# Optimization experiments

Measured on AMD Instinct MI355X. Metric: run time of the kernel, lower is better.

The kernel has to match this reference:

```python
import jax, jax.numpy as jnp
import numpy as np
from jax import lax

EPS_ACT = 1e-5
EPS_RMS = 1e-6


def _ste(x, q):
    # straight-through estimator: forward = q, backward = identity
    return x + lax.stop_gradient(q - x)


def _act_quant8(x):
    # per-last-dim symmetric 8-bit activation quantization (BitNet style)
    scale = 127.0 / jnp.clip(jnp.max(jnp.abs(x), axis=-1, keepdims=True), EPS_ACT)
    return jnp.clip(jnp.round(x * scale), -128.0, 127.0) / scale


def _w_quant_8bit(w):
    # per-tensor symmetric 8-bit weight quantization
    scale = 127.0 / jnp.clip(jnp.max(jnp.abs(w)), EPS_ACT)
    return jnp.clip(jnp.round(w * scale), -128.0, 127.0) / scale


def _w_quant_binary(w):
    # per-tensor binary: sign(w) * mean(|w|)
    return jnp.sign(w) * jnp.mean(jnp.abs(w))


def _rmsnorm(x):
    return x * lax.rsqrt(jnp.mean(x * x, axis=-1, keepdims=True) + EPS_RMS)


def _bit_conv(x, w, quant_type, groups):
    xq = _ste(x, _act_quant8(x))
    wq = _ste(w, _w_quant_binary(w) if quant_type == 'Binary' else _w_quant_8bit(w))
    return lax.conv_general_dilated(
        xq, wq, window_strides=(1, 1), padding='VALID',
        feature_group_count=groups,
        dimension_numbers=('NCHW', 'OIHW', 'NCHW'))


def _bit_linear(x, w):
    x = _rmsnorm(x)                       # NormType='RMS' (no learned scale)
    xq = _ste(x, _act_quant8(x))
    wq = _ste(w, _w_quant_binary(w))      # QuantType='Binary', per-tensor
    return xq @ wq.T


def setup_inputs() -> dict:
    key = jax.random.key(0)
    ks = jax.random.split(key, 8)
    B = 8192
    return {
        'x':        jax.random.normal(ks[0], (B, 1, 16, 16), jnp.float32),
        'w_conv1':  jax.random.normal(ks[1], (16, 1, 3, 3),  jnp.float32) * 0.1,
        'w_conv1b': jax.random.normal(ks[2], (16, 16, 3, 3), jnp.float32) * 0.1,
        'w_conv2':  jax.random.normal(ks[3], (96, 1, 12, 12), jnp.float32) * 0.1,
        'w_fc1':    jax.random.normal(ks[4], (64, 96), jnp.float32) * 0.1,
        'w_fc2':    jax.random.normal(ks[5], (64, 64), jnp.float32) * 0.1,
        'w_fc3':    jax.random.normal(ks[6], (64, 64), jnp.float32) * 0.1,
        'w_fcl':    jax.random.normal(ks[7], (10, 64), jnp.float32) * 0.1,
    }


def reference(x, w_conv1, w_conv1b, w_conv2, w_fc1, w_fc2, w_fc3, w_fcl):
    h = jax.nn.relu(_bit_conv(x, w_conv1, '8bit', 1))        # [B,16,14,14]
    h = jax.nn.relu(_bit_conv(h, w_conv1b, '8bit', 1))       # [B,16,12,12]
    h = jax.nn.relu(_bit_conv(h, w_conv2, 'Binary', 16))     # [B,96,1,1]
    h = h.reshape(h.shape[0], -1)                            # [B,96]
    h = jax.nn.relu(_bit_linear(h, w_fc1))                   # [B,64]
    h = jax.nn.relu(_bit_linear(h, w_fc2))                   # [B,64]
    h = jax.nn.relu(_bit_linear(h, w_fc3))                   # [B,64]
    return _bit_linear(h, w_fcl)                             # [B,10]
```

## Files before the change

kernel.cpp:

```cpp
#include <hip/hip_runtime.h>
#include <math.h>


#define OFF_W1   0
#define OFF_W1B  192
#define OFF_W2   3264
#define OFF_F1   17088
#define OFF_F2   23232
#define OFF_F3   27328
#define OFF_FL   31424

#define EPS_TIE  3e-5f

__device__ __forceinline__ float quantq(float v, float s) {
    const float u  = __fmul_rn(v, s);
    const float fl = floorf(u);
    const float fr = __fsub_rn(u, fl);
    float q;
    if (fabsf(__fsub_rn(fr, 0.5f)) < EPS_TIE) q = __fadd_rn(fl, 0.5f);
    else                                      q = rintf(u);
    q = fminf(q, 127.f);
    return __fdiv_rn(q, s);
}

__device__ __forceinline__ float leaf_abs_sum(const float* __restrict__ p, int n) {
    float r[8];
    #pragma unroll
    for (int j = 0; j < 8; ++j) r[j] = fabsf(p[j]);
    const int nb = n & ~7;
    for (int i = 8; i < nb; i += 8) {
        #pragma unroll
        for (int j = 0; j < 8; ++j) r[j] = __fadd_rn(r[j], fabsf(p[i + j]));
    }
    float c = __fadd_rn(__fadd_rn(__fadd_rn(r[0], r[1]), __fadd_rn(r[2], r[3])),
                        __fadd_rn(__fadd_rn(r[4], r[5]), __fadd_rn(r[6], r[7])));
    for (int i = nb; i < n; ++i) c = __fadd_rn(c, fabsf(p[i]));
    return c;
}

__global__ __launch_bounds__(256) void wq_kernel(
    const float* __restrict__ w1, const float* __restrict__ w1b,
    const float* __restrict__ w2, const float* __restrict__ f1,
    const float* __restrict__ f2, const float* __restrict__ f3,
    const float* __restrict__ fl, float* __restrict__ ws)
{
    __shared__ float red[256];
    __shared__ float ls[128];
    const int blk = blockIdx.x, t = threadIdx.x;

    const float* src; int n; int mode; int off; int K; int W;
    switch (blk) {
        case 0:  src = w1;  n = 144;   mode = 0; off = OFF_W1;  K = 0;   W = 0;  break;
        case 1:  src = w1b; n = 2304;  mode = 0; off = OFF_W1B; K = 0;   W = 0;  break;
        case 2:  src = w2;  n = 13824; mode = 1; off = OFF_W2;  K = 144; W = 96; break;
        case 3:  src = f1;  n = 6144;  mode = 1; off = OFF_F1;  K = 96;  W = 64; break;
        case 4:  src = f2;  n = 4096;  mode = 1; off = OFF_F2;  K = 64;  W = 64; break;
        case 5:  src = f3;  n = 4096;  mode = 1; off = OFF_F3;  K = 64;  W = 64; break;
        default: src = fl;  n = 640;   mode = 1; off = OFF_FL;  K = 64;  W = 10; break;
    }

    if (mode == 0) {
        float p = 0.f;
        for (int i = t; i < n; i += 256) p = fmaxf(p, fabsf(src[i]));
        red[t] = p;
        __syncthreads();
        for (int s = 128; s > 0; s >>= 1) {
            if (t < s) red[t] = fmaxf(red[t], red[t + s]);
            __syncthreads();
        }
        const float s = __fdiv_rn(127.0f, fmaxf(red[0], 1e-5f));
        for (int i = t; i < n; i += 256) {
            float q = rintf(__fmul_rn(src[i], s));
            q = fminf(fmaxf(q, -128.f), 127.f);
            int d;
            if (blk == 0) d = (i / 9) * 12 + (i % 9);
            else          { const int oc = i / 144, k = i % 144;
                            d = oc * 192 + (k / 9) * 12 + (k % 9); }
            ws[off + d] = __fdiv_rn(q, s);
        }
    } else {
        int nleaf, loff, lsz;
        switch (n) {
            case 13824: nleaf = 128; loff = (t >> 1) * 216 + (t & 1) * 104;
                        lsz = (t & 1) ? 112 : 104; break;
            case 6144:  nleaf = 64;  loff = t * 96;  lsz = 96;  break;
            case 4096:  nleaf = 32;  loff = t * 128; lsz = 128; break;
            default:    nleaf = 8;   loff = t * 80;  lsz = 80;  break;
        }
        if (t < nleaf) ls[t] = leaf_abs_sum(src + loff, lsz);
        __syncthreads();
        for (int m = nleaf >> 1; m >= 1; m >>= 1) {
            float v = 0.f;
            if (t < m) v = __fadd_rn(ls[2 * t], ls[2 * t + 1]);
            __syncthreads();
            if (t < m) ls[t] = v;
            __syncthreads();
        }
        const float alpha = __fdiv_rn(ls[0], (float)n);
        for (int i = t; i < n; i += 256) {
            const float w = src[i];
            const float sg = (w > 0.f) ? 1.f : ((w < 0.f) ? -1.f : 0.f);
            const int d = (i % K) * W + (i / K);
            ws[off + d] = __fmul_rn(sg, alpha);
        }
    }
}

__global__ __launch_bounds__(256, 8) void fused_kernel(
    const float* __restrict__ x, const float* __restrict__ ws,
    float* __restrict__ out)
{
    __shared__ __align__(16) float s_x[16][20];
    __shared__ __align__(16) float s_h1[16][14][20];
    __shared__ float s_h2[16 * 156];
    __shared__ float s_v96[96];
    __shared__ float s_t96[96];
    __shared__ float s_q[96];
    __shared__ float s_r8[8];

    const int b = blockIdx.x;
    const int t = threadIdx.x;

    {
        const float v = x[b * 256 + t];
        float m = fabsf(v);
        #pragma unroll
        for (int msk = 8; msk >= 1; msk >>= 1) m = fmaxf(m, __shfl_xor(m, msk, 16));
        const float s = __fdiv_rn(127.0f, fmaxf(m, 1e-5f));
        float q = rintf(__fmul_rn(v, s));
        q = fminf(fmaxf(q, -128.f), 127.f);
        s_x[t >> 4][t & 15] = __fdiv_rn(q, s);
    }
    __syncthreads();

    if (t < 224) {
        const int oc = t / 14, oh = t % 14;
        const float* __restrict__ wg = ws + OFF_W1 + oc * 12;
        const float4 wv0 = *(const float4*)&wg[0];
        const float4 wv1 = *(const float4*)&wg[4];
        const float  w8  = wg[8];
        const float wr[9] = {wv0.x, wv0.y, wv0.z, wv0.w,
                             wv1.x, wv1.y, wv1.z, wv1.w, w8};
        float acc[14];
        #pragma unroll
        for (int ow = 0; ow < 14; ++ow) acc[ow] = 0.f;
        #pragma unroll
        for (int kh = 0; kh < 3; ++kh) {
            float A[16];
            *(float4*)&A[0]  = *(const float4*)&s_x[oh + kh][0];
            *(float4*)&A[4]  = *(const float4*)&s_x[oh + kh][4];
            *(float4*)&A[8]  = *(const float4*)&s_x[oh + kh][8];
            *(float4*)&A[12] = *(const float4*)&s_x[oh + kh][12];
            #pragma unroll
            for (int kw = 0; kw < 3; ++kw) {
                const float wk = wr[kh * 3 + kw];
                #pragma unroll
                for (int ow = 0; ow < 14; ++ow)
                    acc[ow] = __fmaf_rn(A[ow + kw], wk, acc[ow]);
            }
        }
        float mx = 0.f;
        #pragma unroll
        for (int ow = 0; ow < 14; ++ow) { acc[ow] = fmaxf(acc[ow], 0.f); mx = fmaxf(mx, acc[ow]); }
        const float s = __fdiv_rn(127.0f, fmaxf(mx, 1e-5f));
        float q[14];
        #pragma unroll
        for (int ow = 0; ow < 14; ++ow) q[ow] = quantq(acc[ow], s);
        *(float4*)&s_h1[oc][oh][0]  = *(const float4*)&q[0];
        *(float4*)&s_h1[oc][oh][4]  = *(const float4*)&q[4];
        *(float4*)&s_h1[oc][oh][8]  = *(const float4*)&q[8];
        *(float2*)&s_h1[oc][oh][12] = *(const float2*)&q[12];
    }
    __syncthreads();

    if (t < 192) {
        const int oc = t / 12, oh = t % 12;
        const float* __restrict__ wg = ws + OFF_W1B + oc * 192;
        float acc[12];
        #pragma unroll
        for (int i = 0; i < 12; ++i) acc[i] = 0.f;
        for (int ic = 0; ic < 16; ++ic) {
            const float4 wv0 = *(const float4*)&wg[ic * 12];
            const float4 wv1 = *(const float4*)&wg[ic * 12 + 4];
            const float  w8  = wg[ic * 12 + 8];
            const float wr[9] = {wv0.x, wv0.y, wv0.z, wv0.w,
                                 wv1.x, wv1.y, wv1.z, wv1.w, w8};
            #pragma unroll
            for (int kh = 0; kh < 3; ++kh) {
                float A[14];
                *(float4*)&A[0]  = *(const float4*)&s_h1[ic][oh + kh][0];
                *(float4*)&A[4]  = *(const float4*)&s_h1[ic][oh + kh][4];
                *(float4*)&A[8]  = *(const float4*)&s_h1[ic][oh + kh][8];
                *(float2*)&A[12] = *(const float2*)&s_h1[ic][oh + kh][12];
                #pragma unroll
                for (int kw = 0; kw < 3; ++kw) {
                    const float w = wr[kh * 3 + kw];
                    #pragma unroll
                    for (int ow = 0; ow < 12; ++ow)
                        acc[ow] = __fmaf_rn(A[ow + kw], w, acc[ow]);
                }
            }
        }
        float mx = 0.f;
        #pragma unroll
        for (int ow = 0; ow < 12; ++ow) { acc[ow] = fmaxf(acc[ow], 0.f); mx = fmaxf(mx, acc[ow]); }
        const float s = __fdiv_rn(127.0f, fmaxf(mx, 1e-5f));
        const int hb = oc * 156 + oh * 13;
        #pragma unroll
        for (int ow = 0; ow < 12; ++ow)
            s_h2[hb + ow] = quantq(acc[ow], s);
    }
    __syncthreads();

    if (t < 96) {
        const int g = t / 6;
        const float* __restrict__ wp = ws + OFF_W2;
        float acc = 0.f;
        #pragma unroll
        for (int r = 0; r < 12; ++r) {
            const int hb = g * 156 + r * 13;
            #pragma unroll
            for (int c = 0; c < 12; ++c)
                acc = __fmaf_rn(s_h2[hb + c], wp[(r * 12 + c) * 96 + t], acc);
        }
        s_v96[t] = fmaxf(acc, 0.f);
    }
    __syncthreads();

    if (t >= 64) return;

    float u;
    {
        const float va = s_v96[t];
        const float vb = (t < 32) ? s_v96[64 + t] : 0.f;
        s_t96[t] = __fmul_rn(va, va);
        if (t < 32) s_t96[64 + t] = __fmul_rn(vb, vb);
        if (t < 8) {
            float r = s_t96[t];
            for (int i = 8; i < 96; i += 8) r = __fadd_rn(r, s_t96[i + t]);
            s_r8[t] = r;
        }
        const float c = __fadd_rn(
            __fadd_rn(__fadd_rn(s_r8[0], s_r8[1]), __fadd_rn(s_r8[2], s_r8[3])),
            __fadd_rn(__fadd_rn(s_r8[4], s_r8[5]), __fadd_rn(s_r8[6], s_r8[7])));
        const float mean = __fdiv_rn(c, 96.0f);
        const float bc1 = __fdiv_rn(1.0f, __fsqrt_rn(__fadd_rn(mean, 1e-6f)));
        const float n0 = __fmul_rn(va, bc1);
        const float n1 = __fmul_rn(vb, bc1);
        float m = n0;
        if (t < 32) m = fmaxf(m, n1);
        #pragma unroll
        for (int msk = 32; msk >= 1; msk >>= 1) m = fmaxf(m, __shfl_xor(m, msk, 64));
        const float s2 = __fdiv_rn(127.0f, fmaxf(m, 1e-5f));
        s_q[t] = quantq(n0, s2);
        if (t < 32) s_q[64 + t] = quantq(n1, s2);
        const float* __restrict__ wp = ws + OFF_F1;
        float acc = 0.f;
        for (int k = 0; k < 96; ++k) acc = __fmaf_rn(s_q[k], wp[k * 64 + t], acc);
        u = fmaxf(acc, 0.f);
    }

    #pragma unroll 1
    for (int stage = 0; stage < 2; ++stage) {
        const int woff = stage == 0 ? OFF_F2 : OFF_F3;
        s_t96[t] = __fmul_rn(u, u);
        if (t < 8) {
            float r = s_t96[t];
            for (int i = 8; i < 64; i += 8) r = __fadd_rn(r, s_t96[i + t]);
            s_r8[t] = r;
        }
        const float c = __fadd_rn(
            __fadd_rn(__fadd_rn(s_r8[0], s_r8[1]), __fadd_rn(s_r8[2], s_r8[3])),
            __fadd_rn(__fadd_rn(s_r8[4], s_r8[5]), __fadd_rn(s_r8[6], s_r8[7])));
        const float mean = __fdiv_rn(c, 64.0f);
        const float bc1 = __fdiv_rn(1.0f, __fsqrt_rn(__fadd_rn(mean, 1e-6f)));
        const float n0 = __fmul_rn(u, bc1);
        float m = n0;
        #pragma unroll
        for (int msk = 32; msk >= 1; msk >>= 1) m = fmaxf(m, __shfl_xor(m, msk, 64));
        const float s2 = __fdiv_rn(127.0f, fmaxf(m, 1e-5f));
        s_q[t] = quantq(n0, s2);
        const float* __restrict__ wp = ws + woff;
        float acc = 0.f;
        for (int k = 0; k < 64; ++k) acc = __fmaf_rn(s_q[k], wp[k * 64 + t], acc);
        u = fmaxf(acc, 0.f);
    }

    {
        s_t96[t] = __fmul_rn(u, u);
        if (t < 8) {
            float r = s_t96[t];
            for (int i = 8; i < 64; i += 8) r = __fadd_rn(r, s_t96[i + t]);
            s_r8[t] = r;
        }
        const float c = __fadd_rn(
            __fadd_rn(__fadd_rn(s_r8[0], s_r8[1]), __fadd_rn(s_r8[2], s_r8[3])),
            __fadd_rn(__fadd_rn(s_r8[4], s_r8[5]), __fadd_rn(s_r8[6], s_r8[7])));
        const float mean = __fdiv_rn(c, 64.0f);
        const float bc1 = __fdiv_rn(1.0f, __fsqrt_rn(__fadd_rn(mean, 1e-6f)));
        const float n0 = __fmul_rn(u, bc1);
        float m = n0;
        #pragma unroll
        for (int msk = 32; msk >= 1; msk >>= 1) m = fmaxf(m, __shfl_xor(m, msk, 64));
        const float s2 = __fdiv_rn(127.0f, fmaxf(m, 1e-5f));
        s_q[t] = quantq(n0, s2);
        const int to = (t < 10) ? t : 9;
        const float* __restrict__ wp = ws + OFF_FL;
        float acc = 0.f;
        for (int k = 0; k < 64; ++k) acc = __fmaf_rn(s_q[k], wp[k * 10 + to], acc);
        if (t < 10) out[b * 10 + t] = acc;
    }
}

extern "C" void kernel_launch(void* const* d_in, const int* in_sizes, int n_in,
                              void* d_out, int out_size, void* d_ws, size_t ws_size,
                              hipStream_t stream) {
    const float* x   = (const float*)d_in[0];
    const float* w1  = (const float*)d_in[1];
    const float* w1b = (const float*)d_in[2];
    const float* w2  = (const float*)d_in[3];
    const float* f1  = (const float*)d_in[4];
    const float* f2  = (const float*)d_in[5];
    const float* f3  = (const float*)d_in[6];
    const float* fl  = (const float*)d_in[7];
    float* out = (float*)d_out;
    float* ws  = (float*)d_ws;

    const int B = in_sizes[0] / 256;

    wq_kernel<<<7, 256, 0, stream>>>(w1, w1b, w2, f1, f2, f3, fl, ws);
    fused_kernel<<<B, 256, 0, stream>>>(x, ws, out);
}
```

Baseline: 252.7 us.

## Process three images per block and run the MLP tail on three wavefronts

Each block now loops over three images through the conv stages, keeping one 96-wide conv output per image in shared memory. The four-layer MLP tail then runs with one wavefront per image, so three of the four wavefronts are busy instead of one and the idle tail shrinks. The cost is that the conv stages run serially inside each block, the grid has a third as many blocks, and there is more shared memory per block.

```diff
diff --git a/kernel.cpp b/kernel.cpp
--- a/kernel.cpp
+++ b/kernel.cpp
@@ -108,170 +108,180 @@
 
 __global__ __launch_bounds__(256, 8) void fused_kernel(
     const float* __restrict__ x, const float* __restrict__ ws,
-    float* __restrict__ out)
+    float* __restrict__ out, int nimg)
 {
     __shared__ __align__(16) float s_x[16][20];
     __shared__ __align__(16) float s_h1[16][14][20];
     __shared__ float s_h2[16 * 156];
-    __shared__ float s_v96[96];
-    __shared__ float s_t96[96];
-    __shared__ float s_q[96];
-    __shared__ float s_r8[8];
-
-    const int b = blockIdx.x;
+    __shared__ float s_v96[3][96];
+    __shared__ float s_t96[3][96];
+    __shared__ float s_q[3][96];
+    __shared__ float s_r8[3][8];
+
+    const int img0 = blockIdx.x * 3;
     const int t = threadIdx.x;
 
-    {
-        const float v = x[b * 256 + t];
-        float m = fabsf(v);
-        #pragma unroll
-        for (int msk = 8; msk >= 1; msk >>= 1) m = fmaxf(m, __shfl_xor(m, msk, 16));
-        const float s = __fdiv_rn(127.0f, fmaxf(m, 1e-5f));
-        float q = rintf(__fmul_rn(v, s));
-        q = fminf(fmaxf(q, -128.f), 127.f);
-        s_x[t >> 4][t & 15] = __fdiv_rn(q, s);
-    }
-    __syncthreads();
-
-    if (t < 224) {
-        const int oc = t / 14, oh = t % 14;
-        const float* __restrict__ wg = ws + OFF_W1 + oc * 12;
-        const float4 wv0 = *(const float4*)&wg[0];
-        const float4 wv1 = *(const float4*)&wg[4];
-        const float  w8  = wg[8];
-        const float wr[9] = {wv0.x, wv0.y, wv0.z, wv0.w,
-                             wv1.x, wv1.y, wv1.z, wv1.w, w8};
-        float acc[14];
-        #pragma unroll
-        for (int ow = 0; ow < 14; ++ow) acc[ow] = 0.f;
-        #pragma unroll
-        for (int kh = 0; kh < 3; ++kh) {
-            float A[16];
-            *(float4*)&A[0]  = *(const float4*)&s_x[oh + kh][0];
-            *(float4*)&A[4]  = *(const float4*)&s_x[oh + kh][4];
-            *(float4*)&A[8]  = *(const float4*)&s_x[oh + kh][8];
-            *(float4*)&A[12] = *(const float4*)&s_x[oh + kh][12];
-            #pragma unroll
-            for (int kw = 0; kw < 3; ++kw) {
-                const float wk = wr[kh * 3 + kw];
-                #pragma unroll
-                for (int ow = 0; ow < 14; ++ow)
-                    acc[ow] = __fmaf_rn(A[ow + kw], wk, acc[ow]);
-            }
-        }
-        float mx = 0.f;
-        #pragma unroll
-        for (int ow = 0; ow < 14; ++ow) { acc[ow] = fmaxf(acc[ow], 0.f); mx = fmaxf(mx, acc[ow]); }
-        const float s = __fdiv_rn(127.0f, fmaxf(mx, 1e-5f));
-        float q[14];
-        #pragma unroll
-        for (int ow = 0; ow < 14; ++ow) q[ow] = quantq(acc[ow], s);
-        *(float4*)&s_h1[oc][oh][0]  = *(const float4*)&q[0];
-        *(float4*)&s_h1[oc][oh][4]  = *(const float4*)&q[4];
-        *(float4*)&s_h1[oc][oh][8]  = *(const float4*)&q[8];
-        *(float2*)&s_h1[oc][oh][12] = *(const float2*)&q[12];
-    }
-    __syncthreads();
-
-    if (t < 192) {
-        const int oc = t / 12, oh = t % 12;
-        const float* __restrict__ wg = ws + OFF_W1B + oc * 192;
-        float acc[12];
-        #pragma unroll
-        for (int i = 0; i < 12; ++i) acc[i] = 0.f;
-        for (int ic = 0; ic < 16; ++ic) {
-            const float4 wv0 = *(const float4*)&wg[ic * 12];
-            const float4 wv1 = *(const float4*)&wg[ic * 12 + 4];
-            const float  w8  = wg[ic * 12 + 8];
+    #pragma unroll 1
+    for (int im = 0; im < 3; ++im) {
+        const int img = img0 + im;
+        const bool ok = (img < nimg);
+
+        if (ok) {
+            const float v = x[img * 256 + t];
+            float m = fabsf(v);
+            #pragma unroll
+            for (int msk = 8; msk >= 1; msk >>= 1) m = fmaxf(m, __shfl_xor(m, msk, 16));
+            const float s = __fdiv_rn(127.0f, fmaxf(m, 1e-5f));
+            float q = rintf(__fmul_rn(v, s));
+            q = fminf(fmaxf(q, -128.f), 127.f);
+            s_x[t >> 4][t & 15] = __fdiv_rn(q, s);
+        }
+        __syncthreads();
+
+        if (ok && t < 224) {
+            const int oc = t / 14, oh = t % 14;
+            const float* __restrict__ wg = ws + OFF_W1 + oc * 12;
+            const float4 wv0 = *(const float4*)&wg[0];
+            const float4 wv1 = *(const float4*)&wg[4];
+            const float  w8  = wg[8];
             const float wr[9] = {wv0.x, wv0.y, wv0.z, wv0.w,
                                  wv1.x, wv1.y, wv1.z, wv1.w, w8};
+            float acc[14];
+            #pragma unroll
+            for (int ow = 0; ow < 14; ++ow) acc[ow] = 0.f;
             #pragma unroll
             for (int kh = 0; kh < 3; ++kh) {
-                float A[14];
-                *(float4*)&A[0]  = *(const float4*)&s_h1[ic][oh + kh][0];
-                *(float4*)&A[4]  = *(const float4*)&s_h1[ic][oh + kh][4];
-                *(float4*)&A[8]  = *(const float4*)&s_h1[ic][oh + kh][8];
-                *(float2*)&A[12] = *(const float2*)&s_h1[ic][oh + kh][12];
+                float A[16];
+                *(float4*)&A[0]  = *(const float4*)&s_x[oh + kh][0];
+                *(float4*)&A[4]  = *(const float4*)&s_x[oh + kh][4];
+                *(float4*)&A[8]  = *(const float4*)&s_x[oh + kh][8];
+                *(float4*)&A[12] = *(const float4*)&s_x[oh + kh][12];
                 #pragma unroll
                 for (int kw = 0; kw < 3; ++kw) {
-                    const float w = wr[kh * 3 + kw];
+                    const float wk = wr[kh * 3 + kw];
                     #pragma unroll
-                    for (int ow = 0; ow < 12; ++ow)
-                        acc[ow] = __fmaf_rn(A[ow + kw], w, acc[ow]);
+                    for (int ow = 0; ow < 14; ++ow)
+                        acc[ow] = __fmaf_rn(A[ow + kw], wk, acc[ow]);
                 }
             }
-        }
-        float mx = 0.f;
-        #pragma unroll
-        for (int ow = 0; ow < 12; ++ow) { acc[ow] = fmaxf(acc[ow], 0.f); mx = fmaxf(mx, acc[ow]); }
-        const float s = __fdiv_rn(127.0f, fmaxf(mx, 1e-5f));
-        const int hb = oc * 156 + oh * 13;
-        #pragma unroll
-        for (int ow = 0; ow < 12; ++ow)
-            s_h2[hb + ow] = quantq(acc[ow], s);
-    }
-    __syncthreads();
-
-    if (t < 96) {
-        const int g = t / 6;
-        const float* __restrict__ wp = ws + OFF_W2;
-        float acc = 0.f;
-        #pragma unroll
-        for (int r = 0; r < 12; ++r) {
-            const int hb = g * 156 + r * 13;
-            #pragma unroll
-            for (int c = 0; c < 12; ++c)
-                acc = __fmaf_rn(s_h2[hb + c], wp[(r * 12 + c) * 96 + t], acc);
-        }
-        s_v96[t] = fmaxf(acc, 0.f);
-    }
-    __syncthreads();
-
-    if (t >= 64) return;
+            float mx = 0.f;
+            #pragma unroll
+            for (int ow = 0; ow < 14; ++ow) { acc[ow] = fmaxf(acc[ow], 0.f); mx = fmaxf(mx, acc[ow]); }
+            const float s = __fdiv_rn(127.0f, fmaxf(mx, 1e-5f));
+            float q[14];
+            #pragma unroll
+            for (int ow = 0; ow < 14; ++ow) q[ow] = quantq(acc[ow], s);
+            *(float4*)&s_h1[oc][oh][0]  = *(const float4*)&q[0];
+            *(float4*)&s_h1[oc][oh][4]  = *(const float4*)&q[4];
+            *(float4*)&s_h1[oc][oh][8]  = *(const float4*)&q[8];
+            *(float2*)&s_h1[oc][oh][12] = *(const float2*)&q[12];
+        }
+        __syncthreads();
+
+        if (ok && t < 192) {
+            const int oc = t / 12, oh = t % 12;
+            const float* __restrict__ wg = ws + OFF_W1B + oc * 192;
+            float acc[12];
+            #pragma unroll
+            for (int i = 0; i < 12; ++i) acc[i] = 0.f;
+            for (int ic = 0; ic < 16; ++ic) {
+                const float4 wv0 = *(const float4*)&wg[ic * 12];
+                const float4 wv1 = *(const float4*)&wg[ic * 12 + 4];
+                const float  w8  = wg[ic * 12 + 8];
+                const float wr[9] = {wv0.x, wv0.y, wv0.z, wv0.w,
+                                     wv1.x, wv1.y, wv1.z, wv1.w, w8};
+                #pragma unroll
+                for (int kh = 0; kh < 3; ++kh) {
+                    float A[14];
+                    *(float4*)&A[0]  = *(const float4*)&s_h1[ic][oh + kh][0];
+                    *(float4*)&A[4]  = *(const float4*)&s_h1[ic][oh + kh][4];
+                    *(float4*)&A[8]  = *(const float4*)&s_h1[ic][oh + kh][8];
+                    *(float2*)&A[12] = *(const float2*)&s_h1[ic][oh + kh][12];
+                    #pragma unroll
+                    for (int kw = 0; kw < 3; ++kw) {
+                        const float w = wr[kh * 3 + kw];
+                        #pragma unroll
+                        for (int ow = 0; ow < 12; ++ow)
+                            acc[ow] = __fmaf_rn(A[ow + kw], w, acc[ow]);
+                    }
+                }
+            }
+            float mx = 0.f;
+            #pragma unroll
+            for (int ow = 0; ow < 12; ++ow) { acc[ow] = fmaxf(acc[ow], 0.f); mx = fmaxf(mx, acc[ow]); }
+            const float s = __fdiv_rn(127.0f, fmaxf(mx, 1e-5f));
+            const int hb = oc * 156 + oh * 13;
+            #pragma unroll
+            for (int ow = 0; ow < 12; ++ow)
+                s_h2[hb + ow] = quantq(acc[ow], s);
+        }
+        __syncthreads();
+
+        if (ok && t < 96) {
+            const int g = t / 6;
+            const float* __restrict__ wp = ws + OFF_W2;
+            float acc = 0.f;
+            #pragma unroll
+            for (int r = 0; r < 12; ++r) {
+                const int hb = g * 156 + r * 13;
+                #pragma unroll
+                for (int c = 0; c < 12; ++c)
+                    acc = __fmaf_rn(s_h2[hb + c], wp[(r * 12 + c) * 96 + t], acc);
+            }
+            s_v96[im][t] = fmaxf(acc, 0.f);
+        }
+        __syncthreads();
+    }
+
+    const int w = t >> 6;
+    const int l = t & 63;
+    if (w >= 3) return;
+    const int img = img0 + w;
+    if (img >= nimg) return;
 
     float u;
     {
-        const float va = s_v96[t];
-        const float vb = (t < 32) ? s_v96[64 + t] : 0.f;
-        s_t96[t] = __fmul_rn(va, va);
-        if (t < 32) s_t96[64 + t] = __fmul_rn(vb, vb);
-        if (t < 8) {
-            float r = s_t96[t];
-            for (int i = 8; i < 96; i += 8) r = __fadd_rn(r, s_t96[i + t]);
-            s_r8[t] = r;
+        const float va = s_v96[w][l];
+        const float vb = (l < 32) ? s_v96[w][64 + l] : 0.f;
+        s_t96[w][l] = __fmul_rn(va, va);
+        if (l < 32) s_t96[w][64 + l] = __fmul_rn(vb, vb);
+        if (l < 8) {
+            float r = s_t96[w][l];
+            for (int i = 8; i < 96; i += 8) r = __fadd_rn(r, s_t96[w][i + l]);
+            s_r8[w][l] = r;
         }
         const float c = __fadd_rn(
-            __fadd_rn(__fadd_rn(s_r8[0], s_r8[1]), __fadd_rn(s_r8[2], s_r8[3])),
-            __fadd_rn(__fadd_rn(s_r8[4], s_r8[5]), __fadd_rn(s_r8[6], s_r8[7])));
+            __fadd_rn(__fadd_rn(s_r8[w][0], s_r8[w][1]), __fadd_rn(s_r8[w][2], s_r8[w][3])),
+            __fadd_rn(__fadd_rn(s_r8[w][4], s_r8[w][5]), __fadd_rn(s_r8[w][6], s_r8[w][7])));
         const float mean = __fdiv_rn(c, 96.0f);
         const float bc1 = __fdiv_rn(1.0f, __fsqrt_rn(__fadd_rn(mean, 1e-6f)));
         const float n0 = __fmul_rn(va, bc1);
         const float n1 = __fmul_rn(vb, bc1);
         float m = n0;
-        if (t < 32) m = fmaxf(m, n1);
+        if (l < 32) m = fmaxf(m, n1);
         #pragma unroll
         for (int msk = 32; msk >= 1; msk >>= 1) m = fmaxf(m, __shfl_xor(m, msk, 64));
         const float s2 = __fdiv_rn(127.0f, fmaxf(m, 1e-5f));
-        s_q[t] = quantq(n0, s2);
-        if (t < 32) s_q[64 + t] = quantq(n1, s2);
+        s_q[w][l] = quantq(n0, s2);
+        if (l < 32) s_q[w][64 + l] = quantq(n1, s2);
         const float* __restrict__ wp = ws + OFF_F1;
         float acc = 0.f;
-        for (int k = 0; k < 96; ++k) acc = __fmaf_rn(s_q[k], wp[k * 64 + t], acc);
+        for (int k = 0; k < 96; ++k) acc = __fmaf_rn(s_q[w][k], wp[k * 64 + l], acc);
         u = fmaxf(acc, 0.f);
     }
 
     #pragma unroll 1
     for (int stage = 0; stage < 2; ++stage) {
         const int woff = stage == 0 ? OFF_F2 : OFF_F3;
-        s_t96[t] = __fmul_rn(u, u);
-        if (t < 8) {
-            float r = s_t96[t];
-            for (int i = 8; i < 64; i += 8) r = __fadd_rn(r, s_t96[i + t]);
-            s_r8[t] = r;
+        s_t96[w][l] = __fmul_rn(u, u);
+        if (l < 8) {
+            float r = s_t96[w][l];
+            for (int i = 8; i < 64; i += 8) r = __fadd_rn(r, s_t96[w][i + l]);
+            s_r8[w][l] = r;
         }
         const float c = __fadd_rn(
-            __fadd_rn(__fadd_rn(s_r8[0], s_r8[1]), __fadd_rn(s_r8[2], s_r8[3])),
-            __fadd_rn(__fadd_rn(s_r8[4], s_r8[5]), __fadd_rn(s_r8[6], s_r8[7])));
+            __fadd_rn(__fadd_rn(s_r8[w][0], s_r8[w][1]), __fadd_rn(s_r8[w][2], s_r8[w][3])),
+            __fadd_rn(__fadd_rn(s_r8[w][4], s_r8[w][5]), __fadd_rn(s_r8[w][6], s_r8[w][7])));
         const float mean = __fdiv_rn(c, 64.0f);
         const float bc1 = __fdiv_rn(1.0f, __fsqrt_rn(__fadd_rn(mean, 1e-6f)));
         const float n0 = __fmul_rn(u, bc1);
@@ -279,23 +289,23 @@
         #pragma unroll
         for (int msk = 32; msk >= 1; msk >>= 1) m = fmaxf(m, __shfl_xor(m, msk, 64));
         const float s2 = __fdiv_rn(127.0f, fmaxf(m, 1e-5f));
-        s_q[t] = quantq(n0, s2);
+        s_q[w][l] = quantq(n0, s2);
         const float* __restrict__ wp = ws + woff;
         float acc = 0.f;
-        for (int k = 0; k < 64; ++k) acc = __fmaf_rn(s_q[k], wp[k * 64 + t], acc);
+        for (int k = 0; k < 64; ++k) acc = __fmaf_rn(s_q[w][k], wp[k * 64 + l], acc);
         u = fmaxf(acc, 0.f);
     }
 
     {
-        s_t96[t] = __fmul_rn(u, u);
-        if (t < 8) {
-            float r = s_t96[t];
-            for (int i = 8; i < 64; i += 8) r = __fadd_rn(r, s_t96[i + t]);
-            s_r8[t] = r;
+        s_t96[w][l] = __fmul_rn(u, u);
+        if (l < 8) {
+            float r = s_t96[w][l];
+            for (int i = 8; i < 64; i += 8) r = __fadd_rn(r, s_t96[w][i + l]);
+            s_r8[w][l] = r;
         }
         const float c = __fadd_rn(
-            __fadd_rn(__fadd_rn(s_r8[0], s_r8[1]), __fadd_rn(s_r8[2], s_r8[3])),
-            __fadd_rn(__fadd_rn(s_r8[4], s_r8[5]), __fadd_rn(s_r8[6], s_r8[7])));
+            __fadd_rn(__fadd_rn(s_r8[w][0], s_r8[w][1]), __fadd_rn(s_r8[w][2], s_r8[w][3])),
+            __fadd_rn(__fadd_rn(s_r8[w][4], s_r8[w][5]), __fadd_rn(s_r8[w][6], s_r8[w][7])));
         const float mean = __fdiv_rn(c, 64.0f);
         const float bc1 = __fdiv_rn(1.0f, __fsqrt_rn(__fadd_rn(mean, 1e-6f)));
         const float n0 = __fmul_rn(u, bc1);
@@ -303,12 +313,12 @@
         #pragma unroll
         for (int msk = 32; msk >= 1; msk >>= 1) m = fmaxf(m, __shfl_xor(m, msk, 64));
         const float s2 = __fdiv_rn(127.0f, fmaxf(m, 1e-5f));
-        s_q[t] = quantq(n0, s2);
-        const int to = (t < 10) ? t : 9;
+        s_q[w][l] = quantq(n0, s2);
+        const int to = (l < 10) ? l : 9;
         const float* __restrict__ wp = ws + OFF_FL;
         float acc = 0.f;
-        for (int k = 0; k < 64; ++k) acc = __fmaf_rn(s_q[k], wp[k * 10 + to], acc);
-        if (t < 10) out[b * 10 + t] = acc;
+        for (int k = 0; k < 64; ++k) acc = __fmaf_rn(s_q[w][k], wp[k * 10 + to], acc);
+        if (l < 10) out[img * 10 + l] = acc;
     }
 }
 
@@ -327,7 +337,8 @@
     float* ws  = (float*)d_ws;
 
     const int B = in_sizes[0] / 256;
+    const int nblk = (B + 2) / 3;
 
     wq_kernel<<<7, 256, 0, stream>>>(w1, w1b, w2, f1, f2, f3, fl, ws);
-    fused_kernel<<<B, 256, 0, stream>>>(x, ws, out);
-}
+    fused_kernel<<<nblk, 256, 0, stream>>>(x, ws, out, B);
+}
```

Result: slower. 813.7 us (+222.0%).
